# Optimization experiments

Hardware: AMD Instinct MI355X
Metric: run time of the kernel (lower is better)

## Reference

```python
import jax, jax.numpy as jnp
import numpy as np

EMBED = 1024
HEADS = 16
HEAD_DIM = EMBED // HEADS
OUT = 1024


def setup_inputs() -> dict:
    key = jax.random.key(0)
    ks = jax.random.split(key, 6)
    x = jax.random.normal(ks[0], (4, 2048, EMBED), dtype=jnp.float32)
    # per-head projection weights, torch Linear convention: [out_features, in_features]
    s = 1.0 / np.sqrt(HEAD_DIM)
    Wv = jax.random.uniform(ks[1], (HEAD_DIM, HEAD_DIM), jnp.float32, -s, s)
    Wk = jax.random.uniform(ks[2], (HEAD_DIM, HEAD_DIM), jnp.float32, -s, s)
    Wq = jax.random.uniform(ks[3], (HEAD_DIM, HEAD_DIM), jnp.float32, -s, s)
    so = 1.0 / np.sqrt(EMBED)
    Wo = jax.random.uniform(ks[4], (OUT, EMBED), jnp.float32, -so, so)
    bo = jax.random.uniform(ks[5], (OUT,), jnp.float32, -so, so)
    return {"x": x, "Wq": Wq, "Wk": Wk, "Wv": Wv, "Wo": Wo, "bo": bo}


def reference(x, Wq, Wk, Wv, Wo, bo):
    N, L, _ = x.shape
    xh = x.reshape(N, L, HEADS, HEAD_DIM)  # nqhd
    q = jnp.einsum('nqhd,ed->nqhe', xh, Wq)
    k = jnp.einsum('nkhd,ed->nkhe', xh, Wk)
    v = jnp.einsum('nkhd,ed->nkhe', xh, Wv)
    # full score matrix [N, H, Q, K], scaled by sqrt(embed_size) as in source
    energy = jnp.einsum('nqhd,nkhd->nhqk', q, k) / np.sqrt(EMBED).astype(np.float32)
    attn = jax.nn.softmax(energy, axis=3)
    out = jnp.einsum('nhqk,nkhd->nqhd', attn, v).reshape(N, L, EMBED)
    return out @ Wo.T + bo
```

## Files before the change

### kernel.cpp

```cpp
#include <hip/hip_runtime.h>
#include <hip/hip_bf16.h>
#include <stdint.h>
#include <stddef.h>


typedef __attribute__((ext_vector_type(8))) short bf16x8;
typedef __attribute__((ext_vector_type(4))) float f32x4;
typedef __attribute__((ext_vector_type(4))) short short4v;
typedef __attribute__((ext_vector_type(2))) uint32_t uint2v;

__device__ __forceinline__ f32x4 mfma16(bf16x8 a, bf16x8 b, f32x4 c) {
    return __builtin_amdgcn_mfma_f32_16x16x32_bf16(a, b, c, 0, 0, 0);
}

__device__ __forceinline__ short f2bf(float x) {
    union { float f; uint32_t u; } v; v.f = x;
    uint32_t r = (v.u + 0x7FFFu + ((v.u >> 16) & 1u)) >> 16;
    return (short)(uint16_t)r;
}

__device__ __forceinline__ uint32_t pk2bf(float a, float b) {
    union { __hip_bfloat162 h; uint32_t u; } v;
    v.h = __float22bfloat162_rn(float2{a, b});
    return v.u;
}

__device__ __forceinline__ bf16x8 cvt8(const float* __restrict__ p) {
    f32x4 a = *(const f32x4*)p;
    f32x4 b = *(const f32x4*)(p + 4);
    bf16x8 r;
    r[0] = f2bf(a[0]); r[1] = f2bf(a[1]); r[2] = f2bf(a[2]); r[3] = f2bf(a[3]);
    r[4] = f2bf(b[0]); r[5] = f2bf(b[1]); r[6] = f2bf(b[2]); r[7] = f2bf(b[3]);
    return r;
}

__global__ __launch_bounds__(256)
void kvproj_kernel(const float* __restrict__ x, const float* __restrict__ Wk,
                   const float* __restrict__ Wv, short* __restrict__ kf_ws,
                   short* __restrict__ vf_ws) {
    __shared__ alignas(16) short kbuf[128 * 72];
    __shared__ alignas(16) short vbuf[64 * 136];
    int tid = threadIdx.x;
    int lt = blockIdx.x & 15, nh = blockIdx.x >> 4;
    int n = nh >> 4, h = nh & 15;
    int l0 = lt * 128, kt0 = lt * 2;
    int wv = tid >> 6, lane = tid & 63, quad = lane >> 4, lc = lane & 15;

    for (int u = tid; u < 1024; u += 256) {
        int r = u >> 3, c = (u & 7) * 8;
        *(bf16x8*)(kbuf + r * 72 + c) =
            cvt8(x + (size_t)(n * 2048 + l0 + r) * 1024 + h * 64 + c);
    }
    __syncthreads();

    bf16x8 xa[2][2];
    for (int mt = 0; mt < 2; ++mt)
        for (int kf = 0; kf < 2; ++kf)
            xa[mt][kf] = *(bf16x8*)(kbuf + (wv * 32 + mt * 16 + lc) * 72 + kf * 32 + quad * 8);

    f32x4 ka[2][4] = {}, va[2][4] = {};
    for (int nt = 0; nt < 4; ++nt)
        for (int kf = 0; kf < 2; ++kf) {
            bf16x8 wkb = cvt8(Wk + (nt * 16 + lc) * 64 + kf * 32 + quad * 8);
            bf16x8 wvb = cvt8(Wv + (nt * 16 + lc) * 64 + kf * 32 + quad * 8);
            for (int mt = 0; mt < 2; ++mt) {
                ka[mt][nt] = mfma16(xa[mt][kf], wkb, ka[mt][nt]);
                va[mt][nt] = mfma16(xa[mt][kf], wvb, va[mt][nt]);
            }
        }

    for (int mt = 0; mt < 2; ++mt) {
        int off = wv * 32 + mt * 16;
        for (int nt = 0; nt < 4; ++nt) {
            short4v pv;
            for (int i = 0; i < 4; ++i) {
                kbuf[(off + quad * 4 + i) * 72 + nt * 16 + lc] = f2bf(ka[mt][nt][i]);
                pv[i] = f2bf(va[mt][nt][i]);
            }
            *(short4v*)(vbuf + (nt * 16 + lc) * 136 + off + quad * 4) = pv;
        }
    }
    __syncthreads();

    size_t base = (size_t)nh * 131072 + (size_t)kt0 * 4096;
    for (int u = tid; u < 1024; u += 256) {
        int tile = u >> 9, rem = u & 511, seg = rem >> 6, ln = u & 63;
        int t = seg >> 1, kf = seg & 1;
        int lq = ln >> 4, ll = ln & 15;
        bf16x8 kw = *(bf16x8*)(kbuf + (tile * 64 + t * 16 + ll) * 72 + kf * 32 + lq * 8);
        *(bf16x8*)(kf_ws + base + (size_t)tile * 4096 + seg * 512 + ln * 8) = kw;
        bf16x8 vw = *(bf16x8*)(vbuf + (t * 16 + ll) * 136 + tile * 64 + kf * 32 + lq * 8);
        *(bf16x8*)(vf_ws + base + (size_t)tile * 4096 + seg * 512 + ln * 8) = vw;
    }
}

__global__ __launch_bounds__(256, 2)
void flash_kernel(const float* __restrict__ x, const float* __restrict__ Wq,
                  const short* __restrict__ kf_ws, const short* __restrict__ vf_ws,
                  short* __restrict__ ao) {
    __shared__ alignas(16) short pbuf[256 * 72];
    int tid = threadIdx.x;
    int nh = blockIdx.x & 63, qt = blockIdx.x >> 6;
    int n = nh >> 4, h = nh & 15;
    int q0 = qt * 256;
    int wv = tid >> 6, lane = tid & 63, quad = lane >> 4, lc = lane & 15;

    for (int u = tid; u < 2048; u += 256) {
        int r = u >> 3, c = (u & 7) * 8;
        *(bf16x8*)(pbuf + r * 72 + c) =
            cvt8(x + (size_t)(n * 2048 + q0 + r) * 1024 + h * 64 + c);
    }
    __syncthreads();
    {
        bf16x8 xa[4][2];
        for (int mt = 0; mt < 4; ++mt)
            for (int kf = 0; kf < 2; ++kf)
                xa[mt][kf] = *(bf16x8*)(pbuf + (wv * 64 + mt * 16 + lc) * 72 +
                                        kf * 32 + quad * 8);
        f32x4 qacc[4][4] = {};
        for (int nt = 0; nt < 4; ++nt)
            for (int kf = 0; kf < 2; ++kf) {
                bf16x8 wb = cvt8(Wq + (nt * 16 + lc) * 64 + kf * 32 + quad * 8);
                for (int mt = 0; mt < 4; ++mt)
                    qacc[mt][nt] = mfma16(xa[mt][kf], wb, qacc[mt][nt]);
            }
        const float QS = 0.04508422002778011f;
        for (int mt = 0; mt < 4; ++mt)
            for (int nt = 0; nt < 4; ++nt)
                for (int i = 0; i < 4; ++i)
                    pbuf[(wv * 64 + mt * 16 + quad * 4 + i) * 72 + nt * 16 + lc] =
                        f2bf(qacc[mt][nt][i] * QS);
    }
    bf16x8 qa[4][2];
    for (int mt = 0; mt < 4; ++mt)
        for (int kf = 0; kf < 2; ++kf)
            qa[mt][kf] = *(bf16x8*)(pbuf + (wv * 64 + mt * 16 + lc) * 72 +
                                    kf * 32 + quad * 8);

    f32x4 o[4][4] = {};
    float lsum[4] = {0.f, 0.f, 0.f, 0.f};
    const short* kbase = kf_ws + (size_t)nh * 131072 + lane * 8;
    const short* vbase = vf_ws + (size_t)nh * 131072 + lane * 8;

    for (int kt = 0; kt < 32; ++kt) {
        const short* kp = kbase + (size_t)kt * 4096;
        const short* vp = vbase + (size_t)kt * 4096;
        bf16x8 kA[4][2];
#pragma unroll
        for (int t = 0; t < 4; ++t)
            for (int kf = 0; kf < 2; ++kf)
                kA[t][kf] = *(const bf16x8*)(kp + (t * 2 + kf) * 512);
        f32x4 s[4][4] = {};
#pragma unroll
        for (int t = 0; t < 4; ++t)
            for (int q2 = 0; q2 < 4; ++q2) {
                s[q2][t] = mfma16(kA[t][0], qa[q2][0], s[q2][t]);
                s[q2][t] = mfma16(kA[t][1], qa[q2][1], s[q2][t]);
            }
        bf16x8 vA[4][2];
#pragma unroll
        for (int dt = 0; dt < 4; ++dt)
            for (int kf = 0; kf < 2; ++kf)
                vA[dt][kf] = *(const bf16x8*)(vp + (dt * 2 + kf) * 512);
#pragma unroll
        for (int q2 = 0; q2 < 4; ++q2) {
            int prow = (wv * 64 + q2 * 16 + lc) * 72;
            float ts = 0.f;
#pragma unroll
            for (int t = 0; t < 4; ++t) {
                float p0 = __builtin_amdgcn_exp2f(s[q2][t][0]);
                float p1 = __builtin_amdgcn_exp2f(s[q2][t][1]);
                float p2 = __builtin_amdgcn_exp2f(s[q2][t][2]);
                float p3 = __builtin_amdgcn_exp2f(s[q2][t][3]);
                ts += (p0 + p1) + (p2 + p3);
                uint2v w = {pk2bf(p0, p1), pk2bf(p2, p3)};
                *(uint2v*)(pbuf + prow + t * 16 + quad * 4) = w;
            }
            lsum[q2] += ts;
        }
#pragma unroll
        for (int q2 = 0; q2 < 4; ++q2)
            for (int kf = 0; kf < 2; ++kf) {
                bf16x8 pB = *(bf16x8*)(pbuf + (wv * 64 + q2 * 16 + lc) * 72 +
                                       kf * 32 + quad * 8);
                for (int dt = 0; dt < 4; ++dt)
                    o[q2][dt] = mfma16(vA[dt][kf], pB, o[q2][dt]);
            }
    }

    for (int q2 = 0; q2 < 4; ++q2) {
        float t = lsum[q2];
        t += __shfl_xor(t, 16, 64);
        t += __shfl_xor(t, 32, 64);
        float inv = 1.f / t;
        int mtile = (n * 2048 + q0) / 16 + wv * 4 + q2;
        for (int dt = 0; dt < 4; ++dt) {
            int kseg = h * 2 + (dt >> 1);
            int qd8 = ((dt & 1) * 4 + quad) >> 1;
            short4v pk;
            for (int i = 0; i < 4; ++i) pk[i] = f2bf(o[q2][dt][i] * inv);
            *(short4v*)(ao + (size_t)(mtile * 32 + kseg) * 512 +
                        (qd8 * 16 + lc) * 8 + (quad & 1) * 4) = pk;
        }
    }
}

__global__ __launch_bounds__(256)
void wopack_kernel(const float* __restrict__ Wo, short* __restrict__ wfb) {
    int idx = blockIdx.x * 256 + threadIdx.x;
    int nrow = idx >> 7;
    int k0 = (idx & 127) * 8;
    bf16x8 v = cvt8(Wo + (size_t)nrow * 1024 + k0);
    int ntile = nrow >> 4, lcn = nrow & 15;
    int kseg = k0 >> 5, qd = (k0 >> 3) & 3;
    *(bf16x8*)(wfb + ((size_t)(ntile * 32 + kseg) * 64 + qd * 16 + lcn) * 8) = v;
}

__global__ __launch_bounds__(256)
void outgemm_kernel(const short* __restrict__ afb, const short* __restrict__ wfb,
                    const float* __restrict__ bo, float* __restrict__ out) {
    int tid = threadIdx.x;
    int bm = blockIdx.x & 63, bn = blockIdx.x >> 6;
    int m0 = bm * 128, n0 = bn * 128;
    int wv = tid >> 6, lane = tid & 63, quad = lane >> 4, lc = lane & 15;
    int wr = wv >> 1, wc = wv & 1;
    int mtb = bm * 8 + wr * 4;
    int ntb = bn * 8 + wc * 4;

    const short* ab = afb + lane * 8;
    const short* bb = wfb + lane * 8;

    f32x4 acc[4][4] = {};
    for (int kt = 0; kt < 32; ++kt) {
        bf16x8 af[4], bfr[4];
#pragma unroll
        for (int mt = 0; mt < 4; ++mt)
            af[mt] = *(const bf16x8*)(ab + ((size_t)(mtb + mt) * 32 + kt) * 512);
#pragma unroll
        for (int nt = 0; nt < 4; ++nt)
            bfr[nt] = *(const bf16x8*)(bb + ((size_t)(ntb + nt) * 32 + kt) * 512);
#pragma unroll
        for (int mt = 0; mt < 4; ++mt)
            for (int nt = 0; nt < 4; ++nt)
                acc[mt][nt] = mfma16(af[mt], bfr[nt], acc[mt][nt]);
    }
    for (int nt = 0; nt < 4; ++nt) {
        float bv = bo[n0 + wc * 64 + nt * 16 + lc];
        for (int mt = 0; mt < 4; ++mt)
            for (int i = 0; i < 4; ++i) {
                int m = m0 + wr * 64 + mt * 16 + quad * 4 + i;
                int nn = n0 + wc * 64 + nt * 16 + lc;
                out[(size_t)m * 1024 + nn] = acc[mt][nt][i] + bv;
            }
    }
}

extern "C" void kernel_launch(void* const* d_in, const int* in_sizes, int n_in,
                              void* d_out, int out_size, void* d_ws, size_t ws_size,
                              hipStream_t stream) {
    const float* x  = (const float*)d_in[0];
    const float* Wq = (const float*)d_in[1];
    const float* Wk = (const float*)d_in[2];
    const float* Wv = (const float*)d_in[3];
    const float* Wo = (const float*)d_in[4];
    const float* bo = (const float*)d_in[5];
    float* out = (float*)d_out;

    short* kf_ws = (short*)d_ws;
    short* vf_ws = kf_ws + 8388608;
    short* ao_ws = vf_ws + 8388608;
    short* wf_ws = kf_ws;

    kvproj_kernel<<<dim3(1024), dim3(256), 0, stream>>>(x, Wk, Wv, kf_ws, vf_ws);
    flash_kernel<<<dim3(512), dim3(256), 0, stream>>>(x, Wq, kf_ws, vf_ws, ao_ws);
    wopack_kernel<<<dim3(512), dim3(256), 0, stream>>>(Wo, wf_ws);
    outgemm_kernel<<<dim3(512), dim3(256), 0, stream>>>(ao_ws, wf_ws, bo, out);
}
```

Before: 223.8 us.

## Prepack all weights up front and halve flash query tile to double grid

Merges the Wo packing and new Wq/Wk/Wv bf16 fragment packing into one kernel launched first, so kvproj and flash load prepacked bf16 weight fragments instead of converting fp32 weights per block. The flash kernel now handles 128 queries per block instead of 256, doubling the grid to 1024 blocks. It also drops the launch_bounds occupancy hint. This aims for better CU occupancy and load balance, at the cost of re-streaming K/V twice as often per head.

```diff
diff --git a/kernel.cpp b/kernel.cpp
--- a/kernel.cpp
+++ b/kernel.cpp
@@ -35,9 +35,33 @@
 }
 
 __global__ __launch_bounds__(256)
-void kvproj_kernel(const float* __restrict__ x, const float* __restrict__ Wk,
-                   const float* __restrict__ Wv, short* __restrict__ kf_ws,
-                   short* __restrict__ vf_ws) {
+void wpack_kernel(const float* __restrict__ Wo, const float* __restrict__ Wq,
+                  const float* __restrict__ Wk, const float* __restrict__ Wv,
+                  short* __restrict__ wo_f, short* __restrict__ wqkv_f) {
+    int b = blockIdx.x;
+    if (b < 512) {
+        int idx = b * 256 + threadIdx.x;
+        int nrow = idx >> 7;
+        int k0 = (idx & 127) * 8;
+        bf16x8 v = cvt8(Wo + (size_t)nrow * 1024 + k0);
+        int ntile = nrow >> 4, lcn = nrow & 15;
+        int kseg = k0 >> 5, qd = (k0 >> 3) & 3;
+        *(bf16x8*)(wo_f + ((size_t)(ntile * 32 + kseg) * 64 + qd * 16 + lcn) * 8) = v;
+    } else {
+        const float* W = (b == 512) ? Wq : (b == 513) ? Wk : Wv;
+        short* dst = wqkv_f + (size_t)(b - 512) * 4096;
+        for (int u = threadIdx.x; u < 512; u += 256) {
+            int seg = u >> 6, ln = u & 63;
+            int nt = seg >> 1, kf = seg & 1, lq = ln >> 4, lcn = ln & 15;
+            bf16x8 v = cvt8(W + (nt * 16 + lcn) * 64 + kf * 32 + lq * 8);
+            *(bf16x8*)(dst + u * 8) = v;
+        }
+    }
+}
+
+__global__ __launch_bounds__(256)
+void kvproj_kernel(const float* __restrict__ x, const short* __restrict__ wqkv_f,
+                   short* __restrict__ kf_ws, short* __restrict__ vf_ws) {
     __shared__ alignas(16) short kbuf[128 * 72];
     __shared__ alignas(16) short vbuf[64 * 136];
     int tid = threadIdx.x;
@@ -45,6 +69,8 @@
     int n = nh >> 4, h = nh & 15;
     int l0 = lt * 128, kt0 = lt * 2;
     int wv = tid >> 6, lane = tid & 63, quad = lane >> 4, lc = lane & 15;
+    const short* wkf = wqkv_f + 4096 + lane * 8;
+    const short* wvf = wqkv_f + 8192 + lane * 8;
 
     for (int u = tid; u < 1024; u += 256) {
         int r = u >> 3, c = (u & 7) * 8;
@@ -61,8 +87,8 @@
     f32x4 ka[2][4] = {}, va[2][4] = {};
     for (int nt = 0; nt < 4; ++nt)
         for (int kf = 0; kf < 2; ++kf) {
-            bf16x8 wkb = cvt8(Wk + (nt * 16 + lc) * 64 + kf * 32 + quad * 8);
-            bf16x8 wvb = cvt8(Wv + (nt * 16 + lc) * 64 + kf * 32 + quad * 8);
+            bf16x8 wkb = *(const bf16x8*)(wkf + (nt * 2 + kf) * 512);
+            bf16x8 wvb = *(const bf16x8*)(wvf + (nt * 2 + kf) * 512);
             for (int mt = 0; mt < 2; ++mt) {
                 ka[mt][nt] = mfma16(xa[mt][kf], wkb, ka[mt][nt]);
                 va[mt][nt] = mfma16(xa[mt][kf], wvb, va[mt][nt]);
@@ -94,51 +120,52 @@
     }
 }
 
-__global__ __launch_bounds__(256, 2)
-void flash_kernel(const float* __restrict__ x, const float* __restrict__ Wq,
+__global__ __launch_bounds__(256)
+void flash_kernel(const float* __restrict__ x, const short* __restrict__ wqkv_f,
                   const short* __restrict__ kf_ws, const short* __restrict__ vf_ws,
                   short* __restrict__ ao) {
-    __shared__ alignas(16) short pbuf[256 * 72];
+    __shared__ alignas(16) short pbuf[128 * 72];
     int tid = threadIdx.x;
     int nh = blockIdx.x & 63, qt = blockIdx.x >> 6;
     int n = nh >> 4, h = nh & 15;
-    int q0 = qt * 256;
+    int q0 = qt * 128;
     int wv = tid >> 6, lane = tid & 63, quad = lane >> 4, lc = lane & 15;
 
-    for (int u = tid; u < 2048; u += 256) {
+    for (int u = tid; u < 1024; u += 256) {
         int r = u >> 3, c = (u & 7) * 8;
         *(bf16x8*)(pbuf + r * 72 + c) =
             cvt8(x + (size_t)(n * 2048 + q0 + r) * 1024 + h * 64 + c);
     }
     __syncthreads();
     {
-        bf16x8 xa[4][2];
-        for (int mt = 0; mt < 4; ++mt)
+        const short* wqf = wqkv_f + lane * 8;
+        bf16x8 xa[2][2];
+        for (int mt = 0; mt < 2; ++mt)
             for (int kf = 0; kf < 2; ++kf)
-                xa[mt][kf] = *(bf16x8*)(pbuf + (wv * 64 + mt * 16 + lc) * 72 +
+                xa[mt][kf] = *(bf16x8*)(pbuf + (wv * 32 + mt * 16 + lc) * 72 +
                                         kf * 32 + quad * 8);
-        f32x4 qacc[4][4] = {};
+        f32x4 qacc[2][4] = {};
         for (int nt = 0; nt < 4; ++nt)
             for (int kf = 0; kf < 2; ++kf) {
-                bf16x8 wb = cvt8(Wq + (nt * 16 + lc) * 64 + kf * 32 + quad * 8);
-                for (int mt = 0; mt < 4; ++mt)
+                bf16x8 wb = *(const bf16x8*)(wqf + (nt * 2 + kf) * 512);
+                for (int mt = 0; mt < 2; ++mt)
                     qacc[mt][nt] = mfma16(xa[mt][kf], wb, qacc[mt][nt]);
             }
         const float QS = 0.04508422002778011f;
-        for (int mt = 0; mt < 4; ++mt)
+        for (int mt = 0; mt < 2; ++mt)
             for (int nt = 0; nt < 4; ++nt)
                 for (int i = 0; i < 4; ++i)
-                    pbuf[(wv * 64 + mt * 16 + quad * 4 + i) * 72 + nt * 16 + lc] =
+                    pbuf[(wv * 32 + mt * 16 + quad * 4 + i) * 72 + nt * 16 + lc] =
                         f2bf(qacc[mt][nt][i] * QS);
     }
-    bf16x8 qa[4][2];
-    for (int mt = 0; mt < 4; ++mt)
+    bf16x8 qa[2][2];
+    for (int mt = 0; mt < 2; ++mt)
         for (int kf = 0; kf < 2; ++kf)
-            qa[mt][kf] = *(bf16x8*)(pbuf + (wv * 64 + mt * 16 + lc) * 72 +
+            qa[mt][kf] = *(bf16x8*)(pbuf + (wv * 32 + mt * 16 + lc) * 72 +
                                     kf * 32 + quad * 8);
 
-    f32x4 o[4][4] = {};
-    float lsum[4] = {0.f, 0.f, 0.f, 0.f};
+    f32x4 o[2][4] = {};
+    float lsum[2] = {0.f, 0.f};
     const short* kbase = kf_ws + (size_t)nh * 131072 + lane * 8;
     const short* vbase = vf_ws + (size_t)nh * 131072 + lane * 8;
 
@@ -150,10 +177,10 @@
         for (int t = 0; t < 4; ++t)
             for (int kf = 0; kf < 2; ++kf)
                 kA[t][kf] = *(const bf16x8*)(kp + (t * 2 + kf) * 512);
-        f32x4 s[4][4] = {};
+        f32x4 s[2][4] = {};
 #pragma unroll
         for (int t = 0; t < 4; ++t)
-            for (int q2 = 0; q2 < 4; ++q2) {
+            for (int q2 = 0; q2 < 2; ++q2) {
                 s[q2][t] = mfma16(kA[t][0], qa[q2][0], s[q2][t]);
                 s[q2][t] = mfma16(kA[t][1], qa[q2][1], s[q2][t]);
             }
@@ -163,8 +190,8 @@
             for (int kf = 0; kf < 2; ++kf)
                 vA[dt][kf] = *(const bf16x8*)(vp + (dt * 2 + kf) * 512);
 #pragma unroll
-        for (int q2 = 0; q2 < 4; ++q2) {
-            int prow = (wv * 64 + q2 * 16 + lc) * 72;
+        for (int q2 = 0; q2 < 2; ++q2) {
+            int prow = (wv * 32 + q2 * 16 + lc) * 72;
             float ts = 0.f;
 #pragma unroll
             for (int t = 0; t < 4; ++t) {
@@ -179,21 +206,21 @@
             lsum[q2] += ts;
         }
 #pragma unroll
-        for (int q2 = 0; q2 < 4; ++q2)
+        for (int q2 = 0; q2 < 2; ++q2)
             for (int kf = 0; kf < 2; ++kf) {
-                bf16x8 pB = *(bf16x8*)(pbuf + (wv * 64 + q2 * 16 + lc) * 72 +
+                bf16x8 pB = *(bf16x8*)(pbuf + (wv * 32 + q2 * 16 + lc) * 72 +
                                        kf * 32 + quad * 8);
                 for (int dt = 0; dt < 4; ++dt)
                     o[q2][dt] = mfma16(vA[dt][kf], pB, o[q2][dt]);
             }
     }
 
-    for (int q2 = 0; q2 < 4; ++q2) {
+    for (int q2 = 0; q2 < 2; ++q2) {
         float t = lsum[q2];
         t += __shfl_xor(t, 16, 64);
         t += __shfl_xor(t, 32, 64);
         float inv = 1.f / t;
-        int mtile = (n * 2048 + q0) / 16 + wv * 4 + q2;
+        int mtile = (n * 2048 + q0) / 16 + wv * 2 + q2;
         for (int dt = 0; dt < 4; ++dt) {
             int kseg = h * 2 + (dt >> 1);
             int qd8 = ((dt & 1) * 4 + quad) >> 1;
@@ -203,17 +230,6 @@
                         (qd8 * 16 + lc) * 8 + (quad & 1) * 4) = pk;
         }
     }
-}
-
-__global__ __launch_bounds__(256)
-void wopack_kernel(const float* __restrict__ Wo, short* __restrict__ wfb) {
-    int idx = blockIdx.x * 256 + threadIdx.x;
-    int nrow = idx >> 7;
-    int k0 = (idx & 127) * 8;
-    bf16x8 v = cvt8(Wo + (size_t)nrow * 1024 + k0);
-    int ntile = nrow >> 4, lcn = nrow & 15;
-    int kseg = k0 >> 5, qd = (k0 >> 3) & 3;
-    *(bf16x8*)(wfb + ((size_t)(ntile * 32 + kseg) * 64 + qd * 16 + lcn) * 8) = v;
 }
 
 __global__ __launch_bounds__(256)
@@ -266,13 +282,14 @@
     const float* bo = (const float*)d_in[5];
     float* out = (float*)d_out;
 
-    short* kf_ws = (short*)d_ws;
-    short* vf_ws = kf_ws + 8388608;
-    short* ao_ws = vf_ws + 8388608;
-    short* wf_ws = kf_ws;
-
-    kvproj_kernel<<<dim3(1024), dim3(256), 0, stream>>>(x, Wk, Wv, kf_ws, vf_ws);
-    flash_kernel<<<dim3(512), dim3(256), 0, stream>>>(x, Wq, kf_ws, vf_ws, ao_ws);
-    wopack_kernel<<<dim3(512), dim3(256), 0, stream>>>(Wo, wf_ws);
-    outgemm_kernel<<<dim3(512), dim3(256), 0, stream>>>(ao_ws, wf_ws, bo, out);
-}
+    short* kf_ws   = (short*)d_ws;
+    short* vf_ws   = kf_ws + 8388608;
+    short* ao_ws   = vf_ws + 8388608;
+    short* wo_f    = ao_ws + 8388608;
+    short* wqkv_f  = wo_f + 1048576;
+
+    wpack_kernel<<<dim3(515), dim3(256), 0, stream>>>(Wo, Wq, Wk, Wv, wo_f, wqkv_f);
+    kvproj_kernel<<<dim3(1024), dim3(256), 0, stream>>>(x, wqkv_f, kf_ws, vf_ws);
+    flash_kernel<<<dim3(1024), dim3(256), 0, stream>>>(x, wqkv_f, kf_ws, vf_ws, ao_ws);
+    outgemm_kernel<<<dim3(512), dim3(256), 0, stream>>>(ao_ws, wo_f, bo, out);
+}
```

Result: no change. 222.8 us (-0.4%).
